# Kernel optimization log

Hardware: AMD Instinct MI355X
Metric: run time of the kernel (lower is better)

The kernel has to match this reference:

```python
import jax, jax.numpy as jnp
import numpy as np

D_MODEL = 1024
D_INNER = 2048   # expand * d_model
D_STATE = 128
NGROUPS = 1
HEADDIM = 64
NHEADS = D_INNER // HEADDIM  # 32
D_CONV = 4
CHUNK = 256
EPS = 1e-5


def setup_inputs() -> dict:
    key = jax.random.key(0)
    ks = jax.random.split(key, 6)
    B, L = 2, 2048
    d_in_proj = 2 * D_INNER + 2 * NGROUPS * D_STATE + NHEADS  # 4384
    conv_dim = D_INNER + 2 * NGROUPS * D_STATE                # 2304
    u = jax.random.normal(ks[0], (B, L, D_MODEL), jnp.float32)
    W_in = jax.random.normal(ks[1], (d_in_proj, D_MODEL), jnp.float32) * 0.02
    conv_w = jax.random.normal(ks[2], (conv_dim, D_CONV), jnp.float32) * 0.2
    conv_b = jnp.zeros((conv_dim,), jnp.float32)
    # dt_bias = inverse-softplus of dt ~ LogUniform(1e-3, 1e-1), as in __init__
    dt = jnp.exp(jax.random.uniform(ks[3], (NHEADS,), jnp.float32)
                 * (np.log(0.1) - np.log(0.001)) + np.log(0.001))
    dt_bias = dt + jnp.log(-jnp.expm1(-dt))
    A_log = jnp.log(jax.random.uniform(ks[4], (NHEADS,), jnp.float32,
                                       minval=1.0, maxval=16.0))
    D_param = jnp.ones((NHEADS,), jnp.float32)
    norm_w = jnp.ones((D_INNER,), jnp.float32)
    return dict(u=u, W_in=W_in, conv_w=conv_w, conv_b=conv_b,
                dt_bias=dt_bias, A_log=A_log, D_param=D_param, norm_w=norm_w)


def _segsum(x):
    # x: (..., T) -> (..., T, T); entry [i, s] = sum_{j in (s, i]} x_j, -inf above diag
    T = x.shape[-1]
    csum = jnp.cumsum(x, -1)
    diff = csum[..., :, None] - csum[..., None, :]
    mask = jnp.tril(jnp.ones((T, T), dtype=bool))
    return jnp.where(mask, diff, -jnp.inf)


def reference(u, W_in, conv_w, conv_b, dt_bias, A_log, D_param, norm_w):
    B, L, _ = u.shape
    zxbcdt = u @ W_in.T  # (B, L, 2*d_inner + 2*g*N + H)
    z, xBC, dt = jnp.split(zxbcdt, [D_INNER, 2 * D_INNER + 2 * NGROUPS * D_STATE], axis=-1)

    # fused causal depthwise conv1d + silu
    xp = jnp.pad(xBC, ((0, 0), (D_CONV - 1, 0), (0, 0)))
    xc = conv_b
    for k in range(D_CONV):
        xc = xc + xp[:, k:k + L, :] * conv_w[:, k]
    xBC = jax.nn.silu(xc)

    x, Bm, Cm = jnp.split(xBC, [D_INNER, D_INNER + NGROUPS * D_STATE], axis=-1)
    dt = jax.nn.softplus(dt + dt_bias)          # (B, L, H)
    A = -jnp.exp(A_log)                          # (H,)

    x = x.reshape(B, L, NHEADS, HEADDIM)
    Bh = jnp.repeat(Bm.reshape(B, L, NGROUPS, D_STATE), NHEADS // NGROUPS, axis=2)
    Ch = jnp.repeat(Cm.reshape(B, L, NGROUPS, D_STATE), NHEADS // NGROUPS, axis=2)

    # chunked SSD (Mamba2) scan
    nc = L // CHUNK
    xc_ = x.reshape(B, nc, CHUNK, NHEADS, HEADDIM)
    dtc = dt.reshape(B, nc, CHUNK, NHEADS)
    Bc = Bh.reshape(B, nc, CHUNK, NHEADS, D_STATE)
    Cc = Ch.reshape(B, nc, CHUNK, NHEADS, D_STATE)

    a = jnp.moveaxis(dtc * A, -1, 2)             # (B, nc, H, cs)
    a_cum = jnp.cumsum(a, -1)
    Lmat = jnp.exp(_segsum(a))                   # (B, nc, H, cs, cs), lower-tri decay
    xdt = xc_ * dtc[..., None]                   # (B, nc, cs, H, P)

    # intra-chunk (diagonal blocks)
    Y_diag = jnp.einsum('bclhn,bcshn,bchls,bcshp->bclhp', Cc, Bc, Lmat, xdt)

    # chunk-final states and inter-chunk recurrence
    decay_states = jnp.exp(a_cum[..., -1:] - a_cum)         # (B, nc, H, cs)
    states = jnp.einsum('bclhn,bchl,bclhp->bchpn', Bc, decay_states, xdt)
    chunk_decay = jnp.exp(a_cum[..., -1])                   # (B, nc, H)

    def scan_fn(carry, inp):
        s, d = inp                                           # (B,H,P,N), (B,H)
        return carry * d[..., None, None] + s, carry

    init = jnp.zeros((B, NHEADS, HEADDIM, D_STATE), xdt.dtype)
    _, prev_states = jax.lax.scan(scan_fn, init,
                                  (jnp.moveaxis(states, 1, 0),
                                   jnp.moveaxis(chunk_decay, 1, 0)))
    prev_states = jnp.moveaxis(prev_states, 0, 1)            # (B, nc, H, P, N)

    Y_off = jnp.einsum('bclhn,bchpn,bchl->bclhp', Cc, prev_states, jnp.exp(a_cum))

    Y = (Y_diag + Y_off).reshape(B, L, NHEADS, HEADDIM) + D_param[None, None, :, None] * x
    y = Y.reshape(B, L, D_INNER)

    # gated RMSNorm (norm_before_gate=False: gate first, then normalize)
    g = y * jax.nn.silu(z)
    g = g * jax.lax.rsqrt(jnp.mean(g * g, axis=-1, keepdims=True) + EPS) * norm_w
    return g
```

## Files before the change

### kernel.cpp

```cpp
#include <hip/hip_runtime.h>
#include <cstdint>
#include <cmath>

#define KDIM    1024
#define DPROJ   4384
#define NPAD    4480
#define CONVDIM 2304
#define SEQ     2048
#define BATCH   2
#define MROWS   4096
#define NHEADS  32
#define HEADDIM 64
#define DSTATE  128
#define CHUNK   256
#define NCHUNK  8
#define DINNER  2048
#define EPS     1e-5f

typedef unsigned short u16;
typedef float  f32x4  __attribute__((ext_vector_type(4)));
typedef __bf16 bf16x8 __attribute__((ext_vector_type(8)));
typedef u16    u16x8  __attribute__((ext_vector_type(8)));
typedef u16    u16x4  __attribute__((ext_vector_type(4)));

__device__ __forceinline__ u16 f2bf(float f){
  unsigned u = __builtin_bit_cast(unsigned, f);
  u += 0x7fffu + ((u >> 16) & 1u);
  return (u16)(u >> 16);
}
__device__ __forceinline__ float bf2f(u16 s){
  unsigned u = ((unsigned)s) << 16;
  return __builtin_bit_cast(float, u);
}
__device__ __forceinline__ void gl_lds16(const void* g, void* l){
  __builtin_amdgcn_global_load_lds((const __attribute__((address_space(1))) void*)g,
                                   (__attribute__((address_space(3))) void*)l, 16, 0, 0);
}
__device__ __forceinline__ float sigmoidf_(float x){ return 1.f / (1.f + expf(-x)); }

__global__ __launch_bounds__(256) void k_cvt(const float* __restrict__ u_in, u16* __restrict__ u_out,
                                             const float* __restrict__ w_in, u16* __restrict__ w_out){
  int bid = blockIdx.x;
  const float* in; u16* out; size_t i; int wpath = 0;
  if(bid < 4096){ in = u_in; out = u_out; i = ((size_t)bid * 256 + threadIdx.x) * 4; }
  else          { in = w_in; out = w_out; i = ((size_t)(bid - 4096) * 256 + threadIdx.x) * 4; wpath = 1; }
  float4 v = make_float4(0.f,0.f,0.f,0.f);
  if(!wpath || (int)(i >> 10) < DPROJ) v = *(const float4*)(in + i);
  unsigned a = (unsigned)f2bf(v.x) | ((unsigned)f2bf(v.y) << 16);
  unsigned b = (unsigned)f2bf(v.z) | ((unsigned)f2bf(v.w) << 16);
  uint2 o; o.x = a; o.y = b;
  *(uint2*)(out + i) = o;
}

__global__ __launch_bounds__(256) void k_gemm(const u16* __restrict__ A, const u16* __restrict__ B,
                                              u16* __restrict__ zq, float* __restrict__ dtraw){
  __shared__ u16 As[128*64];
  __shared__ u16 Bs[128*64];
  int tid = threadIdx.x;
  int gid = blockIdx.x;
  int mG  = gid / (35*8);
  int rem = gid % (35*8);
  int nblk = rem / 8;
  int mblk = mG*8 + (rem & 7);
  int m0 = mblk * 128, n0 = nblk * 128;
  int w = tid >> 6, lane = tid & 63, r = lane & 15, q = lane >> 4;
  int wm = (w >> 1) * 64, wn = (w & 1) * 64;
  f32x4 acc[4][4] = {};
  const u16* Ag = A + (size_t)(m0 + (tid >> 3)) * KDIM + (tid & 7) * 8;
  const u16* Bg = B + (size_t)(n0 + (tid >> 3)) * KDIM + (tid & 7) * 8;
  for(int kt = 0; kt < KDIM/64; kt++){
    int k0 = kt * 64;
    #pragma unroll
    for(int m = 0; m < 4; m++){
      gl_lds16(Ag + (size_t)m*32*KDIM + k0, &As[((size_t)m*256 + tid) * 8]);
      gl_lds16(Bg + (size_t)m*32*KDIM + k0, &Bs[((size_t)m*256 + tid) * 8]);
    }
    __syncthreads();
    #pragma unroll
    for(int ks = 0; ks < 2; ks++){
      bf16x8 af[4], bfm[4];
      #pragma unroll
      for(int i = 0; i < 4; i++) af[i]  = *(const bf16x8*)&As[(wm + i*16 + r) * 64 + ks*32 + q*8];
      #pragma unroll
      for(int j = 0; j < 4; j++) bfm[j] = *(const bf16x8*)&Bs[(wn + j*16 + r) * 64 + ks*32 + q*8];
      #pragma unroll
      for(int i = 0; i < 4; i++)
        #pragma unroll
        for(int j = 0; j < 4; j++)
          acc[i][j] = __builtin_amdgcn_mfma_f32_16x16x32_bf16(af[i], bfm[j], acc[i][j], 0, 0, 0);
    }
    __syncthreads();
  }
  #pragma unroll
  for(int i = 0; i < 4; i++)
    #pragma unroll
    for(int j = 0; j < 4; j++)
      #pragma unroll
      for(int e = 0; e < 4; e++){
        int row = m0 + wm + i*16 + q*4 + e;
        int col = n0 + wn + j*16 + r;
        zq[(size_t)row * NPAD + col] = f2bf(acc[i][j][e]);
        if(nblk == 34) dtraw[(size_t)row * 128 + (col - 4352)] = acc[i][j][e];
      }
}

__global__ __launch_bounds__(256) void k_conv(const u16* __restrict__ zq,
                                              const float* __restrict__ cw,
                                              const float* __restrict__ cb,
                                              u16* __restrict__ xq, u16* __restrict__ xqT,
                                              u16* __restrict__ Bq, u16* __restrict__ Cq){
  int c0 = blockIdx.x * 256;
  int l0 = blockIdx.y * 64;
  int b  = blockIdx.z;
  int tid = threadIdx.x;
  int cbase = c0 + (tid & 63) * 4;
  int lb = l0 + (tid >> 6) * 16;
  float wt[4][4], bias[4];
  #pragma unroll
  for(int cc = 0; cc < 4; cc++){
    float4 wv = *(const float4*)(cw + (cbase + cc)*4);
    wt[cc][0]=wv.x; wt[cc][1]=wv.y; wt[cc][2]=wv.z; wt[cc][3]=wv.w;
    bias[cc] = cb[cbase + cc];
  }
  const u16* zrow = zq + (size_t)(b*SEQ) * NPAD + 2048 + cbase;
  float w0[4] = {}, w1[4] = {}, w2[4] = {};
  if(lb-3 >= 0){ u16x4 v = *(const u16x4*)(zrow + (size_t)(lb-3)*NPAD);
    #pragma unroll
    for(int cc=0;cc<4;cc++) w0[cc] = bf2f(v[cc]); }
  if(lb-2 >= 0){ u16x4 v = *(const u16x4*)(zrow + (size_t)(lb-2)*NPAD);
    #pragma unroll
    for(int cc=0;cc<4;cc++) w1[cc] = bf2f(v[cc]); }
  if(lb-1 >= 0){ u16x4 v = *(const u16x4*)(zrow + (size_t)(lb-1)*NPAD);
    #pragma unroll
    for(int cc=0;cc<4;cc++) w2[cc] = bf2f(v[cc]); }
  u16 vals[16][4];
  #pragma unroll
  for(int rr = 0; rr < 16; rr++){
    u16x4 v = *(const u16x4*)(zrow + (size_t)(lb+rr)*NPAD);
    #pragma unroll
    for(int cc = 0; cc < 4; cc++){
      float in3 = bf2f(v[cc]);
      float a = bias[cc] + w0[cc]*wt[cc][0] + w1[cc]*wt[cc][1] + w2[cc]*wt[cc][2] + in3*wt[cc][3];
      vals[rr][cc] = f2bf(a * sigmoidf_(a));
      w0[cc] = w1[cc]; w1[cc] = w2[cc]; w2[cc] = in3;
    }
  }
  if(blockIdx.x < 8){
    #pragma unroll
    for(int rr = 0; rr < 16; rr++){
      u16x4 o; o[0]=vals[rr][0]; o[1]=vals[rr][1]; o[2]=vals[rr][2]; o[3]=vals[rr][3];
      *(u16x4*)(xq + (size_t)(b*SEQ + lb + rr) * DINNER + cbase) = o;
    }
    #pragma unroll
    for(int cc = 0; cc < 4; cc++){
      int c = cbase + cc;
      int h = c >> 6, p = c & 63;
      u16* dst = xqT + ((size_t)((b*32 + h)*64) + p) * SEQ + lb;
      u16x8 v0, v1;
      #pragma unroll
      for(int m = 0; m < 8; m++){ v0[m] = vals[m][cc]; v1[m] = vals[8+m][cc]; }
      *(u16x8*)dst = v0;
      *(u16x8*)(dst + 8) = v1;
    }
  } else {
    int col = cbase - 2048;
    u16* dst = (col < 128) ? Bq : Cq;
    int c4 = col & 127;
    #pragma unroll
    for(int rr = 0; rr < 16; rr++){
      u16x4 o; o[0]=vals[rr][0]; o[1]=vals[rr][1]; o[2]=vals[rr][2]; o[3]=vals[rr][3];
      *(u16x4*)(dst + (size_t)(b*SEQ + lb + rr) * 128 + c4) = o;
    }
  }
}

__global__ __launch_bounds__(256) void k_acum(const float* __restrict__ dtraw,
                                              const float* __restrict__ dt_bias,
                                              const float* __restrict__ A_log,
                                              float* __restrict__ dtb,
                                              float* __restrict__ acum,
                                              float* __restrict__ cdec){
  int bid = blockIdx.x;
  int h = bid & 31, c = (bid >> 5) & 7, b = bid >> 8;
  int t = threadIdx.x;
  __shared__ float sb[256];
  size_t row = (size_t)(b*SEQ + c*CHUNK + t);
  float v = dtraw[row * 128 + h] + dt_bias[h];
  float dt = (v > 20.f) ? v : log1pf(expf(v));
  dtb[row * 32 + h] = dt;
  float Ah = -expf(A_log[h]);
  float a = dt * Ah;
  sb[t] = a; __syncthreads();
  for(int off = 1; off < 256; off <<= 1){
    float vv = (t >= off) ? sb[t - off] : 0.f;
    __syncthreads();
    sb[t] += vv;
    __syncthreads();
  }
  float ac = sb[t];
  acum[(size_t)bid * 256 + t] = ac;
  if(t == 255) cdec[bid] = expf(ac);
}

__global__ __launch_bounds__(256) void k_states(const u16* __restrict__ xqT, const u16* __restrict__ Bq,
                                                const float* __restrict__ dtb,
                                                const float* __restrict__ acum,
                                                u16* __restrict__ states){
  int bid = blockIdx.x;
  int h = bid & 31, c = (bid >> 5) & 7, b = bid >> 8;
  int tid = threadIdx.x;
  int w = tid >> 6, lane = tid & 63, r = lane & 15, q = lane >> 4;
  __shared__ u16 bT[128*72];
  size_t rowB = (size_t)(b*SEQ + c*CHUNK);
  const u16* xrow = xqT + (size_t)((b*32 + h)*64) * SEQ + c*CHUNK;
  float alast = acum[(size_t)bid * 256 + 255];
  f32x4 acc[4][2] = {};
  for(int slab = 0; slab < 4; slab++){
    int lb = slab * 64;
    int l = lane;
    float f = expf(alast - acum[(size_t)bid * 256 + lb + l]) * dtb[(rowB + lb + l) * 32 + h];
    __syncthreads();
    const u16* bp = Bq + (rowB + lb + l) * 128 + w*32;
    #pragma unroll
    for(int k = 0; k < 4; k++){
      u16x8 v = *(const u16x8*)(bp + k*8);
      #pragma unroll
      for(int m = 0; m < 8; m++)
        bT[(w*32 + k*8 + m)*72 + l] = f2bf(bf2f(v[m]) * f);
    }
    __syncthreads();
    #pragma unroll
    for(int ks = 0; ks < 2; ks++){
      bf16x8 af[4], bfr[2];
      #pragma unroll
      for(int i = 0; i < 4; i++)
        af[i] = *(const bf16x8*)&xrow[(size_t)(i*16 + r) * SEQ + lb + ks*32 + q*8];
      #pragma unroll
      for(int j = 0; j < 2; j++) bfr[j] = *(const bf16x8*)&bT[(w*32 + j*16 + r)*72 + ks*32 + q*8];
      #pragma unroll
      for(int i = 0; i < 4; i++)
        #pragma unroll
        for(int j = 0; j < 2; j++)
          acc[i][j] = __builtin_amdgcn_mfma_f32_16x16x32_bf16(af[i], bfr[j], acc[i][j], 0, 0, 0);
    }
  }
  #pragma unroll
  for(int i = 0; i < 4; i++)
    #pragma unroll
    for(int j = 0; j < 2; j++)
      #pragma unroll
      for(int e = 0; e < 4; e++){
        int p = i*16 + q*4 + e;
        int n = w*32 + j*16 + r;
        states[((size_t)bid * 64 + p) * 128 + n] = f2bf(acc[i][j][e]);
      }
}

__global__ __launch_bounds__(256) void k_scan(const u16* __restrict__ states,
                                              const float* __restrict__ cdec,
                                              u16* __restrict__ prevb){
  size_t i = (size_t)blockIdx.x * 256 + threadIdx.x;
  int n = (int)(i & 127), p = (int)((i >> 7) & 63), h = (int)((i >> 13) & 31), b = (int)(i >> 18);
  float carry = 0.f;
  for(int c = 0; c < NCHUNK; c++){
    int bch = (b*8 + c)*32 + h;
    size_t off = ((size_t)bch * 64 + p) * 128 + n;
    float s = bf2f(states[off]);
    prevb[off] = f2bf(carry);
    carry = carry * cdec[bch] + s;
  }
}

__global__ __launch_bounds__(128) void k_y(const u16* __restrict__ xqT, const u16* __restrict__ Bq,
                                           const u16* __restrict__ Cq, const float* __restrict__ dtb,
                                           const float* __restrict__ acum, const u16* __restrict__ prevb,
                                           u16* __restrict__ yq){
  int bid = blockIdx.x;
  int bch = bid >> 1, pr = bid & 1;
  int h = bch & 31, c = (bch >> 5) & 7, b = bch >> 8;
  int tid = threadIdx.x;
  int w2 = tid >> 6, lane = tid & 63, r = lane & 15, q = lane >> 4;
  int lt = pr ? (1 + w2) : (w2 * 3);
  int l0 = lt * 64;
  __shared__ float acl[256];
  __shared__ float dts[256];
  __shared__ u16 G[2][64*72];
  size_t rowC = (size_t)(b*SEQ + c*CHUNK);
  #pragma unroll
  for(int it = 0; it < 2; it++){
    int s = it*128 + tid;
    acl[s] = acum[(size_t)bch * 256 + s];
    dts[s] = dtb[(rowC + s) * 32 + h];
  }
  __syncthreads();
  bf16x8 cf[4][4];
  #pragma unroll
  for(int i = 0; i < 4; i++)
    #pragma unroll
    for(int ks = 0; ks < 4; ks++)
      cf[i][ks] = *(const bf16x8*)&Cq[(rowC + l0 + i*16 + r) * 128 + ks*32 + q*8];
  f32x4 accY[4][4] = {};
  #pragma unroll
  for(int ks = 0; ks < 4; ks++){
    #pragma unroll
    for(int j = 0; j < 4; j++){
      bf16x8 bfr = *(const bf16x8*)&prevb[((size_t)bch * 64 + j*16 + r) * 128 + ks*32 + q*8];
      #pragma unroll
      for(int i = 0; i < 4; i++)
        accY[i][j] = __builtin_amdgcn_mfma_f32_16x16x32_bf16(cf[i][ks], bfr, accY[i][j], 0, 0, 0);
    }
  }
  #pragma unroll
  for(int i = 0; i < 4; i++)
    #pragma unroll
    for(int e = 0; e < 4; e++){
      float sc = expf(acl[l0 + i*16 + q*4 + e]);
      #pragma unroll
      for(int j = 0; j < 4; j++) accY[i][j][e] *= sc;
    }
  const u16* xrow = xqT + (size_t)((b*32 + h)*64) * SEQ + c*CHUNK;
  u16* Gw = G[w2];
  for(int st = 0; st <= lt; st++){
    int s0 = st * 64;
    f32x4 accS[4][4] = {};
    #pragma unroll
    for(int ks = 0; ks < 4; ks++){
      #pragma unroll
      for(int j = 0; j < 4; j++){
        bf16x8 bfr = *(const bf16x8*)&Bq[(rowC + s0 + j*16 + r) * 128 + ks*32 + q*8];
        #pragma unroll
        for(int i = 0; i < 4; i++)
          accS[i][j] = __builtin_amdgcn_mfma_f32_16x16x32_bf16(cf[i][ks], bfr, accS[i][j], 0, 0, 0);
      }
    }
    #pragma unroll
    for(int i = 0; i < 4; i++)
      #pragma unroll
      for(int j = 0; j < 4; j++)
        #pragma unroll
        for(int e = 0; e < 4; e++){
          int ll = l0 + i*16 + q*4 + e;
          int ss = s0 + j*16 + r;
          float v = (ll >= ss) ? accS[i][j][e] * expf(acl[ll] - acl[ss]) * dts[ss] : 0.f;
          Gw[(i*16 + q*4 + e)*72 + j*16 + r] = f2bf(v);
        }
    #pragma unroll
    for(int ks = 0; ks < 2; ks++){
      bf16x8 gf[4], xf[4];
      #pragma unroll
      for(int i = 0; i < 4; i++) gf[i] = *(const bf16x8*)&Gw[(i*16 + r)*72 + ks*32 + q*8];
      #pragma unroll
      for(int j = 0; j < 4; j++)
        xf[j] = *(const bf16x8*)&xrow[(size_t)(j*16 + r) * SEQ + s0 + ks*32 + q*8];
      #pragma unroll
      for(int i = 0; i < 4; i++)
        #pragma unroll
        for(int j = 0; j < 4; j++)
          accY[i][j] = __builtin_amdgcn_mfma_f32_16x16x32_bf16(gf[i], xf[j], accY[i][j], 0, 0, 0);
    }
  }
  #pragma unroll
  for(int i = 0; i < 4; i++)
    #pragma unroll
    for(int j = 0; j < 4; j++)
      #pragma unroll
      for(int e = 0; e < 4; e++){
        int ll = l0 + i*16 + q*4 + e;
        int p = j*16 + r;
        yq[(rowC + ll) * (size_t)DINNER + h*64 + p] = f2bf(accY[i][j][e]);
      }
}

__global__ __launch_bounds__(256) void k_norm(const u16* __restrict__ yq, const u16* __restrict__ xq,
                                              const u16* __restrict__ zq, const float* __restrict__ Dp,
                                              const float* __restrict__ nw, float* __restrict__ out){
  int bl = blockIdx.x;
  int t = threadIdx.x;
  float Dh = Dp[t >> 3];
  u16x8 yv = *(const u16x8*)(yq + (size_t)bl * DINNER + t*8);
  u16x8 xv = *(const u16x8*)(xq + (size_t)bl * DINNER + t*8);
  u16x8 zv = *(const u16x8*)(zq + (size_t)bl * NPAD + t*8);
  float g[8];
  float ss = 0.f;
  #pragma unroll
  for(int m = 0; m < 8; m++){
    float y = bf2f(yv[m]) + Dh * bf2f(xv[m]);
    float z = bf2f(zv[m]);
    float v = y * (z * sigmoidf_(z));
    g[m] = v;
    ss += v * v;
  }
  #pragma unroll
  for(int off = 32; off > 0; off >>= 1) ss += __shfl_down(ss, off, 64);
  __shared__ float wsum[4];
  if((t & 63) == 0) wsum[t >> 6] = ss;
  __syncthreads();
  float tot = wsum[0] + wsum[1] + wsum[2] + wsum[3];
  float scale = rsqrtf(tot / (float)DINNER + EPS);
  float4 o0, o1;
  o0.x = g[0]*scale*nw[t*8+0]; o0.y = g[1]*scale*nw[t*8+1];
  o0.z = g[2]*scale*nw[t*8+2]; o0.w = g[3]*scale*nw[t*8+3];
  o1.x = g[4]*scale*nw[t*8+4]; o1.y = g[5]*scale*nw[t*8+5];
  o1.z = g[6]*scale*nw[t*8+6]; o1.w = g[7]*scale*nw[t*8+7];
  *(float4*)(out + (size_t)bl * DINNER + t*8)     = o0;
  *(float4*)(out + (size_t)bl * DINNER + t*8 + 4) = o1;
}

extern "C" void kernel_launch(void* const* d_in, const int* in_sizes, int n_in,
                              void* d_out, int out_size, void* d_ws, size_t ws_size,
                              hipStream_t stream){
  const float* u    = (const float*)d_in[0];
  const float* W    = (const float*)d_in[1];
  const float* cw   = (const float*)d_in[2];
  const float* cb   = (const float*)d_in[3];
  const float* dtbi = (const float*)d_in[4];
  const float* Alog = (const float*)d_in[5];
  const float* Dp   = (const float*)d_in[6];
  const float* nw   = (const float*)d_in[7];
  float* out = (float*)d_out;

  char* ws = (char*)d_ws;
  size_t off = 0;
  auto alloc = [&](size_t bytes) -> void* {
    void* p = ws + off;
    off += (bytes + 255) & ~(size_t)255;
    return p;
  };
  u16*   u_bf    = (u16*)  alloc((size_t)MROWS * KDIM * 2);
  u16*   W_bf    = (u16*)  alloc((size_t)NPAD * KDIM * 2);
  u16*   zq      = (u16*)  alloc((size_t)MROWS * NPAD * 2);
  float* dtraw   = (float*)alloc((size_t)MROWS * 128 * 4);
  u16*   xq      = (u16*)  alloc((size_t)MROWS * DINNER * 2);
  u16*   xqT     = (u16*)  alloc((size_t)MROWS * DINNER * 2);
  u16*   Bq      = (u16*)  alloc((size_t)MROWS * 128 * 2);
  u16*   Cq      = (u16*)  alloc((size_t)MROWS * 128 * 2);
  float* dtb     = (float*)alloc((size_t)MROWS * 32 * 4);
  float* acum    = (float*)alloc((size_t)512 * 256 * 4);
  float* cdec    = (float*)alloc((size_t)512 * 4);
  u16*   states  = (u16*)  alloc((size_t)512 * 64 * 128 * 2);
  u16*   prevb   = (u16*)  alloc((size_t)512 * 64 * 128 * 2);
  u16*   yq      = (u16*)  alloc((size_t)MROWS * DINNER * 2);

  k_cvt<<<4096 + 4480, 256, 0, stream>>>(u, u_bf, W, W_bf);
  k_gemm<<<35*32, 256, 0, stream>>>(u_bf, W_bf, zq, dtraw);
  k_conv<<<dim3(9, 32, 2), 256, 0, stream>>>(zq, cw, cb, xq, xqT, Bq, Cq);
  k_acum<<<512, 256, 0, stream>>>(dtraw, dtbi, Alog, dtb, acum, cdec);
  k_states<<<512, 256, 0, stream>>>(xqT, Bq, dtb, acum, states);
  k_scan<<<((size_t)BATCH*NHEADS*64*128)/256, 256, 0, stream>>>(states, cdec, prevb);
  k_y<<<1024, 128, 0, stream>>>(xqT, Bq, Cq, dtb, acum, prevb, yq);
  k_norm<<<MROWS, 256, 0, stream>>>(yq, xq, zq, Dp, nw, out);
}
```

Before: 304.1 us.

## Swizzle GEMM LDS, remap GEMM blocks per XCD, single-wave k_y with exp2

The GEMM now XOR-swizzles LDS column chunks to avoid bank conflicts on fragment reads. It also remaps block IDs so each XCD works on a contiguous M×N region for better L2 reuse, launching padded blocks that exit early. k_y becomes a one-wave-per-block kernel over a single 64-row tile, and the causal mask test is applied only on the diagonal sub-tile. Exponentials are rewritten as exp2f on log2e-prescaled values. Removing the barrier in k_y relies on single-wave execution.

Result: faster. 275.3 us (-9.5%).

```diff
diff --git a/kernel.cpp b/kernel.cpp
--- a/kernel.cpp
+++ b/kernel.cpp
@@ -16,6 +16,7 @@
 #define NCHUNK  8
 #define DINNER  2048
 #define EPS     1e-5f
+#define LOG2E   1.44269504088896f
 
 typedef unsigned short u16;
 typedef float  f32x4  __attribute__((ext_vector_type(4)));
@@ -58,16 +59,18 @@
   __shared__ u16 Bs[128*64];
   int tid = threadIdx.x;
   int gid = blockIdx.x;
-  int mG  = gid / (35*8);
-  int rem = gid % (35*8);
-  int nblk = rem / 8;
-  int mblk = mG*8 + (rem & 7);
+  int xcd = gid & 7, idx = gid >> 3;
+  int xm = xcd >> 2, xn = xcd & 3;
+  int mblk = xm*16 + (idx & 15);
+  int nblk = xn*9  + (idx >> 4);
+  if(nblk >= 35) return;
   int m0 = mblk * 128, n0 = nblk * 128;
   int w = tid >> 6, lane = tid & 63, r = lane & 15, q = lane >> 4;
   int wm = (w >> 1) * 64, wn = (w & 1) * 64;
   f32x4 acc[4][4] = {};
-  const u16* Ag = A + (size_t)(m0 + (tid >> 3)) * KDIM + (tid & 7) * 8;
-  const u16* Bg = B + (size_t)(n0 + (tid >> 3)) * KDIM + (tid & 7) * 8;
+  int cg = (tid & 7) ^ ((tid >> 3) & 7);
+  const u16* Ag = A + (size_t)(m0 + (tid >> 3)) * KDIM + cg * 8;
+  const u16* Bg = B + (size_t)(n0 + (tid >> 3)) * KDIM + cg * 8;
   for(int kt = 0; kt < KDIM/64; kt++){
     int k0 = kt * 64;
     #pragma unroll
@@ -78,11 +81,12 @@
     __syncthreads();
     #pragma unroll
     for(int ks = 0; ks < 2; ks++){
+      int ca = ((ks*4 + q) ^ (r & 7)) * 8;
       bf16x8 af[4], bfm[4];
       #pragma unroll
-      for(int i = 0; i < 4; i++) af[i]  = *(const bf16x8*)&As[(wm + i*16 + r) * 64 + ks*32 + q*8];
-      #pragma unroll
-      for(int j = 0; j < 4; j++) bfm[j] = *(const bf16x8*)&Bs[(wn + j*16 + r) * 64 + ks*32 + q*8];
+      for(int i = 0; i < 4; i++) af[i]  = *(const bf16x8*)&As[(wm + i*16 + r) * 64 + ca];
+      #pragma unroll
+      for(int j = 0; j < 4; j++) bfm[j] = *(const bf16x8*)&Bs[(wn + j*16 + r) * 64 + ca];
       #pragma unroll
       for(int i = 0; i < 4; i++)
         #pragma unroll
@@ -199,7 +203,7 @@
   }
   float ac = sb[t];
   acum[(size_t)bid * 256 + t] = ac;
-  if(t == 255) cdec[bid] = expf(ac);
+  if(t == 255) cdec[bid] = exp2f(ac * LOG2E);
 }
 
 __global__ __launch_bounds__(256) void k_states(const u16* __restrict__ xqT, const u16* __restrict__ Bq,
@@ -218,7 +222,7 @@
   for(int slab = 0; slab < 4; slab++){
     int lb = slab * 64;
     int l = lane;
-    float f = expf(alast - acum[(size_t)bid * 256 + lb + l]) * dtb[(rowB + lb + l) * 32 + h];
+    float f = exp2f((alast - acum[(size_t)bid * 256 + lb + l]) * LOG2E) * dtb[(rowB + lb + l) * 32 + h];
     __syncthreads();
     const u16* bp = Bq + (rowB + lb + l) * 128 + w*32;
     #pragma unroll
@@ -271,28 +275,25 @@
   }
 }
 
-__global__ __launch_bounds__(128) void k_y(const u16* __restrict__ xqT, const u16* __restrict__ Bq,
-                                           const u16* __restrict__ Cq, const float* __restrict__ dtb,
-                                           const float* __restrict__ acum, const u16* __restrict__ prevb,
-                                           u16* __restrict__ yq){
+__global__ __launch_bounds__(64) void k_y(const u16* __restrict__ xqT, const u16* __restrict__ Bq,
+                                          const u16* __restrict__ Cq, const float* __restrict__ dtb,
+                                          const float* __restrict__ acum, const u16* __restrict__ prevb,
+                                          u16* __restrict__ yq){
   int bid = blockIdx.x;
-  int bch = bid >> 1, pr = bid & 1;
+  int lt = bid & 3, bch = bid >> 2;
   int h = bch & 31, c = (bch >> 5) & 7, b = bch >> 8;
-  int tid = threadIdx.x;
-  int w2 = tid >> 6, lane = tid & 63, r = lane & 15, q = lane >> 4;
-  int lt = pr ? (1 + w2) : (w2 * 3);
+  int t = threadIdx.x, r = t & 15, q = t >> 4;
   int l0 = lt * 64;
-  __shared__ float acl[256];
+  __shared__ float acl2[256];
   __shared__ float dts[256];
-  __shared__ u16 G[2][64*72];
+  __shared__ u16 G[64*72];
   size_t rowC = (size_t)(b*SEQ + c*CHUNK);
   #pragma unroll
-  for(int it = 0; it < 2; it++){
-    int s = it*128 + tid;
-    acl[s] = acum[(size_t)bch * 256 + s];
+  for(int it = 0; it < 4; it++){
+    int s = it*64 + t;
+    acl2[s] = acum[(size_t)bch * 256 + s] * LOG2E;
     dts[s] = dtb[(rowC + s) * 32 + h];
   }
-  __syncthreads();
   bf16x8 cf[4][4];
   #pragma unroll
   for(int i = 0; i < 4; i++)
@@ -314,12 +315,11 @@
   for(int i = 0; i < 4; i++)
     #pragma unroll
     for(int e = 0; e < 4; e++){
-      float sc = expf(acl[l0 + i*16 + q*4 + e]);
+      float sc = exp2f(acl2[l0 + i*16 + q*4 + e]);
       #pragma unroll
       for(int j = 0; j < 4; j++) accY[i][j][e] *= sc;
     }
   const u16* xrow = xqT + (size_t)((b*32 + h)*64) * SEQ + c*CHUNK;
-  u16* Gw = G[w2];
   for(int st = 0; st <= lt; st++){
     int s0 = st * 64;
     f32x4 accS[4][4] = {};
@@ -333,22 +333,41 @@
           accS[i][j] = __builtin_amdgcn_mfma_f32_16x16x32_bf16(cf[i][ks], bfr, accS[i][j], 0, 0, 0);
       }
     }
-    #pragma unroll
-    for(int i = 0; i < 4; i++)
-      #pragma unroll
-      for(int j = 0; j < 4; j++)
+    float aS[4], dS[4];
+    #pragma unroll
+    for(int j = 0; j < 4; j++){ aS[j] = acl2[s0 + j*16 + r]; dS[j] = dts[s0 + j*16 + r]; }
+    if(st < lt){
+      #pragma unroll
+      for(int i = 0; i < 4; i++)
         #pragma unroll
         for(int e = 0; e < 4; e++){
-          int ll = l0 + i*16 + q*4 + e;
-          int ss = s0 + j*16 + r;
-          float v = (ll >= ss) ? accS[i][j][e] * expf(acl[ll] - acl[ss]) * dts[ss] : 0.f;
-          Gw[(i*16 + q*4 + e)*72 + j*16 + r] = f2bf(v);
+          float aL = acl2[l0 + i*16 + q*4 + e];
+          #pragma unroll
+          for(int j = 0; j < 4; j++){
+            float v = accS[i][j][e] * exp2f(aL - aS[j]) * dS[j];
+            G[(i*16 + q*4 + e)*72 + j*16 + r] = f2bf(v);
+          }
         }
+    } else {
+      #pragma unroll
+      for(int i = 0; i < 4; i++)
+        #pragma unroll
+        for(int e = 0; e < 4; e++){
+          int ll = i*16 + q*4 + e;
+          float aL = acl2[l0 + ll];
+          #pragma unroll
+          for(int j = 0; j < 4; j++){
+            int ss = j*16 + r;
+            float v = (ll >= ss) ? accS[i][j][e] * exp2f(aL - aS[j]) * dS[j] : 0.f;
+            G[(i*16 + q*4 + e)*72 + j*16 + r] = f2bf(v);
+          }
+        }
+    }
     #pragma unroll
     for(int ks = 0; ks < 2; ks++){
       bf16x8 gf[4], xf[4];
       #pragma unroll
-      for(int i = 0; i < 4; i++) gf[i] = *(const bf16x8*)&Gw[(i*16 + r)*72 + ks*32 + q*8];
+      for(int i = 0; i < 4; i++) gf[i] = *(const bf16x8*)&G[(i*16 + r)*72 + ks*32 + q*8];
       #pragma unroll
       for(int j = 0; j < 4; j++)
         xf[j] = *(const bf16x8*)&xrow[(size_t)(j*16 + r) * SEQ + s0 + ks*32 + q*8];
@@ -442,11 +461,11 @@
   u16*   yq      = (u16*)  alloc((size_t)MROWS * DINNER * 2);
 
   k_cvt<<<4096 + 4480, 256, 0, stream>>>(u, u_bf, W, W_bf);
-  k_gemm<<<35*32, 256, 0, stream>>>(u_bf, W_bf, zq, dtraw);
+  k_gemm<<<1152, 256, 0, stream>>>(u_bf, W_bf, zq, dtraw);
   k_conv<<<dim3(9, 32, 2), 256, 0, stream>>>(zq, cw, cb, xq, xqT, Bq, Cq);
   k_acum<<<512, 256, 0, stream>>>(dtraw, dtbi, Alog, dtb, acum, cdec);
   k_states<<<512, 256, 0, stream>>>(xqT, Bq, dtb, acum, states);
   k_scan<<<((size_t)BATCH*NHEADS*64*128)/256, 256, 0, stream>>>(states, cdec, prevb);
-  k_y<<<1024, 128, 0, stream>>>(xqT, Bq, Cq, dtb, acum, prevb, yq);
+  k_y<<<2048, 64, 0, stream>>>(xqT, Bq, Cq, dtb, acum, prevb, yq);
   k_norm<<<MROWS, 256, 0, stream>>>(yq, xq, zq, Dp, nw, out);
 }
```
